# Performance work log

Hardware: AMD Instinct MI355X
Metric: run time of the kernel (lower is better)

Reference implementation:

```python
import jax, jax.numpy as jnp
import numpy as np

H, W, PART = 16, 16, 4
EPS = 1e-5


def _window_rows(h, part):
    # Static, boundary-clamped window row indices, as in position_aware_max.
    pr = h // part
    half = pr // 2
    idx = []
    for i in range(h):
        u, l = i - half, i + half
        if u < 0:
            u, l = 0, pr
        if l > h:
            u, l = h - pr, h
        idx.append(np.arange(u, l))
    return np.stack(idx)  # [h, pr] (uniform length since pr is even)


def _pam(s6, row_idx, dim):
    # s6: [p, g, hr, wr, hc, wc]; row index r = hr*W + wr, col index s = hc*W + wc.
    if dim == 0:
        # per column block i (hc == i): max over rows hr in window, all wr; keep wc
        sc = jnp.moveaxis(s6, 4, 0)  # [hc, p, g, hr, wr, wc]
        f = lambda sci, idx: jnp.take(sci, idx, axis=2).max(axis=(2, 3))
    else:
        # per row block i (hr == i): max over cols hc in window, all wc; keep wr
        sc = jnp.moveaxis(s6, 2, 0)  # [hr, p, g, wr, hc, wc]
        f = lambda sci, idx: jnp.take(sci, idx, axis=3).max(axis=(3, 4))
    out = jax.vmap(f)(sc, jnp.asarray(row_idx))  # [h, p, g, w]
    p, g = s6.shape[0], s6.shape[1]
    return jnp.transpose(out, (1, 2, 0, 3)).reshape(p, g, -1)  # [p, g, hw]


def _bn(x, gamma, beta, axes):
    # BatchNorm in training mode: biased batch statistics (torch default).
    m = x.mean(axis=axes, keepdims=True)
    v = x.var(axis=axes, keepdims=True)
    return gamma * (x - m) * jax.lax.rsqrt(v + EPS) + beta


def setup_inputs() -> dict:
    key = jax.random.key(0)
    k0, k1, k2 = jax.random.split(key, 3)
    p, g, c = 48, 48, 64
    hw = H * W
    return {
        "prob_fea": jax.random.normal(k0, (p, c, H, W), jnp.float32),
        "gal_fea": jax.random.normal(k1, (g, c, H, W), jnp.float32),
        "bn_gamma": jnp.ones((1,), jnp.float32),
        "bn_beta": jnp.zeros((1,), jnp.float32),
        "fc_w": jnp.full((1, hw), 1.0 / hw, jnp.float32),  # reset_parameters fill
        "fc_b": jax.random.normal(k2, (1,), jnp.float32) * 0.01,
        "lbn_gamma": jnp.ones((1,), jnp.float32),
        "lbn_beta": jnp.zeros((1,), jnp.float32),
    }


def reference(prob_fea, gal_fea, bn_gamma, bn_beta, fc_w, fc_b, lbn_gamma, lbn_beta):
    p, c = prob_fea.shape[0], prob_fea.shape[1]
    g = gal_fea.shape[0]
    hw = H * W
    pf = prob_fea.reshape(p, c, hw)
    gf = gal_fea.reshape(g, c, hw)
    score = jnp.einsum('pcs,gcr->pgrs', pf, gf)  # [p, g, hw, hw]
    s6 = score.reshape(p, g, H, W, H, W)
    row_idx = _window_rows(H, PART)
    s1 = _pam(s6, row_idx, 0)  # [p, g, hw]
    s2 = _pam(s6, row_idx, 1)  # [p, g, hw]
    sc = jnp.concatenate([s1, s2], axis=-1).reshape(-1, 1, hw)  # [2*p*g, 1, hw]
    sc = _bn(sc, bn_gamma, bn_beta, (0, 2)).reshape(-1, hw)
    sc = sc @ fc_w.T + fc_b  # [2*p*g, 1]
    sc = sc.reshape(-1, 2).sum(axis=1, keepdims=True)  # [p*g, 1]
    sc = _bn(sc, lbn_gamma, lbn_beta, (0,))
    return jax.nn.sigmoid(sc).reshape(p, g)
```

## Files before the change

### kernel.cpp

```cpp
#include <hip/hip_runtime.h>

typedef __attribute__((ext_vector_type(8))) short short8;
typedef __attribute__((ext_vector_type(4))) float float4v;

__constant__ unsigned short WIN[16] = {
    0x000F, 0x000F, 0x000F, 0x001E, 0x003C, 0x0078, 0x00F0, 0x01E0,
    0x03C0, 0x0780, 0x0F00, 0x1E00, 0x3C00, 0x7800, 0xF000, 0xF000
};
__constant__ int LO8[8] = {0, 0, 2, 4, 6, 8, 10, 12};
__constant__ int HI8[8] = {3, 5, 7, 9, 11, 13, 15, 15};

__device__ __forceinline__ unsigned short f2bf(float f) {
    unsigned int x = __builtin_bit_cast(unsigned int, f);
    x += 0x7FFF + ((x >> 16) & 1);
    return (unsigned short)(x >> 16);
}

struct __align__(16) U16x8 { unsigned short u[8]; };

__global__ __launch_bounds__(256) void pretranspose_kernel(
    const float* __restrict__ prob,
    const float* __restrict__ gal,
    unsigned short* __restrict__ outT)
{
    const int img = blockIdx.x;
    const float* src = (img < 48) ? (prob + img * 16384)
                                  : (gal + (img - 48) * 16384);
    unsigned short* dst = outT + img * 16384;
    const int tid = threadIdx.x;
    const int c0 = (tid & 7) * 8;
    const int s0 = (tid >> 3) * 8;
    unsigned short v[8][8];
#pragma unroll
    for (int i = 0; i < 8; ++i) {
        const float* p = src + (c0 + i) * 256 + s0;
        const float4v f0 = *(const float4v*)(p);
        const float4v f1 = *(const float4v*)(p + 4);
        v[i][0] = f2bf(f0.x); v[i][1] = f2bf(f0.y);
        v[i][2] = f2bf(f0.z); v[i][3] = f2bf(f0.w);
        v[i][4] = f2bf(f1.x); v[i][5] = f2bf(f1.y);
        v[i][6] = f2bf(f1.z); v[i][7] = f2bf(f1.w);
    }
#pragma unroll
    for (int j = 0; j < 8; ++j) {
        U16x8 o;
#pragma unroll
        for (int i = 0; i < 8; ++i) o.u[i] = v[i][j];
        const int srow = s0 + j;
        const int off = srow * 64 + (((c0 >> 3) ^ (srow & 7)) << 3);
        *(U16x8*)(dst + off) = o;
    }
}

__global__ __launch_bounds__(256, 3) void score_pam_kernel(
    const unsigned short* __restrict__ preT,
    const float* __restrict__ fcw,
    float* __restrict__ outDot,
    float* __restrict__ outSum,
    float* __restrict__ outSq)
{
    __shared__ unsigned short pfT[256 * 64];
    __shared__ unsigned short gfT[128 * 64];
    __shared__ float s1part[4 * 256];
    __shared__ float s2buf[256];

    const int tid = threadIdx.x;
    const int pair = blockIdx.x;
    const int ip = pair / 48;
    const int ig = pair % 48;
    const unsigned short* pimg = preT + ip * 16384;
    const unsigned short* gimg = preT + (48 + ig) * 16384;

    {
        float4v m = { -3.0e38f, -3.0e38f, -3.0e38f, -3.0e38f };
        *(float4v*)(s1part + tid * 4) = m;
    }
#pragma unroll
    for (int j = 0; j < 8; ++j) {
        const int off = j * 2048 + tid * 8;
        *(U16x8*)(pfT + off) = *(const U16x8*)(pimg + off);
    }

    const int lane = tid & 63;
    const int w = tid >> 6;
    const int laneM = lane & 15;
    const int q = lane >> 4;
    const int swzl = laneM & 7;

    for (int phase = 0; phase < 2; ++phase) {
        if (phase) __syncthreads();
#pragma unroll
        for (int j = 0; j < 4; ++j) {
            const int off = j * 2048 + tid * 8;
            *(U16x8*)(gfT + off) = *(const U16x8*)(gimg + phase * 8192 + off);
        }
        __syncthreads();

        const int t = phase * 4 + w;
        const int hr0 = 2 * t;
        const int hr1 = hr0 + 1;
        const int rl0 = 32 * w + laneM;
        const int rl1 = rl0 + 16;
        const short8 a00 = *(const short8*)(gfT + rl0 * 64 + ((q ^ swzl) << 3));
        const short8 a01 = *(const short8*)(gfT + rl0 * 64 + (((q + 4) ^ swzl) << 3));
        const short8 a10 = *(const short8*)(gfT + rl1 * 64 + ((q ^ swzl) << 3));
        const short8 a11 = *(const short8*)(gfT + rl1 * 64 + (((q + 4) ^ swzl) << 3));
        const unsigned int win0 = WIN[hr0];
        const unsigned int win1 = WIN[hr1];
        float4v s2r0 = { -3.0e38f, -3.0e38f, -3.0e38f, -3.0e38f };
        float4v s2r1 = s2r0;
        const int lo = LO8[t], hi = HI8[t];

        int sl = lo * 16 + laneM;
        short8 b0 = *(const short8*)(pfT + sl * 64 + ((q ^ swzl) << 3));
        short8 b1 = *(const short8*)(pfT + sl * 64 + (((q + 4) ^ swzl) << 3));
        for (int hc = lo; hc <= hi; ++hc) {
            const int hcn = (hc < hi) ? hc + 1 : hc;
            const int sln = hcn * 16 + laneM;
            const short8 nb0 = *(const short8*)(pfT + sln * 64 + ((q ^ swzl) << 3));
            const short8 nb1 = *(const short8*)(pfT + sln * 64 + (((q + 4) ^ swzl) << 3));

            float4v acc0 = { 0.f, 0.f, 0.f, 0.f };
            float4v acc1 = acc0;
            acc0 = __builtin_amdgcn_mfma_f32_16x16x32_bf16(a00, b0, acc0, 0, 0, 0);
            acc0 = __builtin_amdgcn_mfma_f32_16x16x32_bf16(a01, b1, acc0, 0, 0, 0);
            acc1 = __builtin_amdgcn_mfma_f32_16x16x32_bf16(a10, b0, acc1, 0, 0, 0);
            acc1 = __builtin_amdgcn_mfma_f32_16x16x32_bf16(a11, b1, acc1, 0, 0, 0);

            const bool s20 = (win0 >> hc) & 1;
            const bool s21 = (win1 >> hc) & 1;
            const unsigned int wc = WIN[hc];
            const bool s10 = (wc >> hr0) & 1;
            const bool s11 = (wc >> hr1) & 1;

            if (s20) {
                s2r0.x = fmaxf(s2r0.x, acc0.x); s2r0.y = fmaxf(s2r0.y, acc0.y);
                s2r0.z = fmaxf(s2r0.z, acc0.z); s2r0.w = fmaxf(s2r0.w, acc0.w);
            }
            if (s21) {
                s2r1.x = fmaxf(s2r1.x, acc1.x); s2r1.y = fmaxf(s2r1.y, acc1.y);
                s2r1.z = fmaxf(s2r1.z, acc1.z); s2r1.w = fmaxf(s2r1.w, acc1.w);
            }
            if (s10 || s11) {
                float vm = -3.0e38f;
                if (s10) vm = fmaxf(fmaxf(acc0.x, acc0.y), fmaxf(acc0.z, acc0.w));
                if (s11) vm = fmaxf(vm, fmaxf(fmaxf(acc1.x, acc1.y),
                                              fmaxf(acc1.z, acc1.w)));
                vm = fmaxf(vm, __shfl_xor(vm, 16, 64));
                vm = fmaxf(vm, __shfl_xor(vm, 32, 64));
                if (lane < 16) {
                    float* p = &s1part[w * 256 + hc * 16 + lane];
                    *p = fmaxf(*p, vm);
                }
            }
            b0 = nb0; b1 = nb1;
        }
#pragma unroll
        for (int d = 1; d < 16; d <<= 1) {
            s2r0.x = fmaxf(s2r0.x, __shfl_xor(s2r0.x, d, 64));
            s2r0.y = fmaxf(s2r0.y, __shfl_xor(s2r0.y, d, 64));
            s2r0.z = fmaxf(s2r0.z, __shfl_xor(s2r0.z, d, 64));
            s2r0.w = fmaxf(s2r0.w, __shfl_xor(s2r0.w, d, 64));
            s2r1.x = fmaxf(s2r1.x, __shfl_xor(s2r1.x, d, 64));
            s2r1.y = fmaxf(s2r1.y, __shfl_xor(s2r1.y, d, 64));
            s2r1.z = fmaxf(s2r1.z, __shfl_xor(s2r1.z, d, 64));
            s2r1.w = fmaxf(s2r1.w, __shfl_xor(s2r1.w, d, 64));
        }
        if (laneM == 0) {
            const int r0 = hr0 * 16 + q * 4;
            s2buf[r0 + 0] = s2r0.x; s2buf[r0 + 1] = s2r0.y;
            s2buf[r0 + 2] = s2r0.z; s2buf[r0 + 3] = s2r0.w;
            const int r1 = hr1 * 16 + q * 4;
            s2buf[r1 + 0] = s2r1.x; s2buf[r1 + 1] = s2r1.y;
            s2buf[r1 + 2] = s2r1.z; s2buf[r1 + 3] = s2r1.w;
        }
    }
    __syncthreads();

    {
        const float s1v = fmaxf(fmaxf(s1part[tid], s1part[256 + tid]),
                                fmaxf(s1part[512 + tid], s1part[768 + tid]));
        const float s2v = s2buf[tid];
        const float wj = fcw[tid];
        float dv = (s1v + s2v) * wj;
        float sv = s1v + s2v;
        float qv = s1v * s1v + s2v * s2v;
#pragma unroll
        for (int d = 32; d >= 1; d >>= 1) {
            dv += __shfl_down(dv, d, 64);
            sv += __shfl_down(sv, d, 64);
            qv += __shfl_down(qv, d, 64);
        }
        __syncthreads();
        if (lane == 0) {
            s2buf[w] = dv; s2buf[8 + w] = sv; s2buf[16 + w] = qv;
        }
        __syncthreads();
        if (tid == 0) {
            outDot[pair] = s2buf[0] + s2buf[1] + s2buf[2] + s2buf[3];
            outSum[pair] = s2buf[8] + s2buf[9] + s2buf[10] + s2buf[11];
            outSq[pair]  = s2buf[16] + s2buf[17] + s2buf[18] + s2buf[19];
        }
    }
}

__global__ __launch_bounds__(256) void finalize_kernel(
    const float* __restrict__ dDot,
    const float* __restrict__ dSum,
    const float* __restrict__ dSq,
    const float* __restrict__ bng,
    const float* __restrict__ bnb,
    const float* __restrict__ fcw,
    const float* __restrict__ fcb,
    const float* __restrict__ lg,
    const float* __restrict__ lb,
    float* __restrict__ outp)
{
    __shared__ float red[12];
    const int tid = threadIdx.x;
    const int lane = tid & 63;
    const int w = tid >> 6;

    float S = 0.f, Q = 0.f;
    float dv[9];
#pragma unroll
    for (int k = 0; k < 9; ++k) {
        const int i = tid + 256 * k;
        dv[k] = dDot[i];
        S += dSum[i];
        Q += dSq[i];
    }
    float Wj = fcw[tid];
#pragma unroll
    for (int d = 32; d >= 1; d >>= 1) {
        S += __shfl_down(S, d, 64);
        Q += __shfl_down(Q, d, 64);
        Wj += __shfl_down(Wj, d, 64);
    }
    if (lane == 0) { red[w] = S; red[4 + w] = Q; red[8 + w] = Wj; }
    __syncthreads();
    S = red[0] + red[1] + red[2] + red[3];
    Q = red[4] + red[5] + red[6] + red[7];
    const float W = red[8] + red[9] + red[10] + red[11];
    __syncthreads();

    const float N1 = 1179648.0f;
    const float m1 = S / N1;
    const float v1 = Q / N1 - m1 * m1;
    const float inv1 = rsqrtf(v1 + 1e-5f);
    const float g1 = bng[0], b1 = bnb[0], fb = fcb[0];
    const float g2 = lg[0], b2 = lb[0];
    const float cA = g1 * inv1;
    const float cB = 2.f * (b1 * W + fb) - cA * 2.f * m1 * W;

    float Sy = 0.f, Qy = 0.f;
    float yv[9];
#pragma unroll
    for (int k = 0; k < 9; ++k) {
        const float y = cA * dv[k] + cB;
        yv[k] = y;
        Sy += y;
        Qy += y * y;
    }
#pragma unroll
    for (int d = 32; d >= 1; d >>= 1) {
        Sy += __shfl_down(Sy, d, 64);
        Qy += __shfl_down(Qy, d, 64);
    }
    if (lane == 0) { red[w] = Sy; red[4 + w] = Qy; }
    __syncthreads();
    Sy = red[0] + red[1] + red[2] + red[3];
    Qy = red[4] + red[5] + red[6] + red[7];

    const float m2 = Sy / 2304.0f;
    const float v2 = Qy / 2304.0f - m2 * m2;
    const float inv2 = rsqrtf(v2 + 1e-5f);
#pragma unroll
    for (int k = 0; k < 9; ++k) {
        const int i = tid + 256 * k;
        const float z = g2 * (yv[k] - m2) * inv2 + b2;
        outp[i] = 1.0f / (1.0f + __expf(-z));
    }
}

extern "C" void kernel_launch(void* const* d_in, const int* in_sizes, int n_in,
                              void* d_out, int out_size, void* d_ws, size_t ws_size,
                              hipStream_t stream) {
    const float* prob = (const float*)d_in[0];
    const float* gal  = (const float*)d_in[1];
    const float* bng  = (const float*)d_in[2];
    const float* bnb  = (const float*)d_in[3];
    const float* fcw  = (const float*)d_in[4];
    const float* fcb  = (const float*)d_in[5];
    const float* lg   = (const float*)d_in[6];
    const float* lb   = (const float*)d_in[7];

    unsigned short* preT = (unsigned short*)d_ws;
    float* ws = (float*)((char*)d_ws + 96 * 16384 * sizeof(unsigned short));
    float* dDot = ws;
    float* dSum = ws + 2304;
    float* dSq  = ws + 4608;

    hipLaunchKernelGGL(pretranspose_kernel, dim3(96), dim3(256), 0, stream,
                       prob, gal, preT);
    hipLaunchKernelGGL(score_pam_kernel, dim3(48 * 48), dim3(256), 0, stream,
                       preT, fcw, dDot, dSum, dSq);
    hipLaunchKernelGGL(finalize_kernel, dim3(1), dim3(256), 0, stream,
                       dDot, dSum, dSq, bng, bnb, fcw, fcb, lg, lb,
                       (float*)d_out);
}
```

Measured before the change: 111.0 us.

## Compute PAM via symmetric two-pass window tiles with DPP row reductions

Restructures the score/PAM kernel so both max directions use the same code path. One pass stages the probe image in LDS and the other stages the gallery image, with A fragments loaded directly from global memory. This replaces the s1 cross-wave LDS partial-max scheme with per-row-tile running maxima. Those maxima are reduced with DPP row operations instead of shuffles, and the fc weights are staged in LDS. LDS use drops and launch bounds rise to 4 blocks per CU, which may recompute some overlapping MFMA tiles and cost registers.

```diff
diff --git a/kernel.cpp b/kernel.cpp
--- a/kernel.cpp
+++ b/kernel.cpp
@@ -3,12 +3,8 @@
 typedef __attribute__((ext_vector_type(8))) short short8;
 typedef __attribute__((ext_vector_type(4))) float float4v;
 
-__constant__ unsigned short WIN[16] = {
-    0x000F, 0x000F, 0x000F, 0x001E, 0x003C, 0x0078, 0x00F0, 0x01E0,
-    0x03C0, 0x0780, 0x0F00, 0x1E00, 0x3C00, 0x7800, 0xF000, 0xF000
-};
-__constant__ int LO8[8] = {0, 0, 2, 4, 6, 8, 10, 12};
-__constant__ int HI8[8] = {3, 5, 7, 9, 11, 13, 15, 15};
+__constant__ int LOW[16] = {0,0,0,1,2,3,4,5,6,7,8,9,10,11,12,12};
+__constant__ int HIW[16] = {3,3,3,4,5,6,7,8,9,10,11,12,13,14,15,15};
 
 __device__ __forceinline__ unsigned short f2bf(float f) {
     unsigned int x = __builtin_bit_cast(unsigned int, f);
@@ -17,6 +13,20 @@
 }
 
 struct __align__(16) U16x8 { unsigned short u[8]; };
+
+template <int CTRL>
+__device__ __forceinline__ float dppmaxf(float x) {
+    int y = __builtin_amdgcn_update_dpp(0, __builtin_bit_cast(int, x),
+                                        CTRL, 0xF, 0xF, true);
+    return fmaxf(x, __builtin_bit_cast(float, y));
+}
+__device__ __forceinline__ float rowmax16(float x) {
+    x = dppmaxf<0xB1>(x);
+    x = dppmaxf<0x4E>(x);
+    x = dppmaxf<0x141>(x);
+    x = dppmaxf<0x140>(x);
+    return x;
+}
 
 __global__ __launch_bounds__(256) void pretranspose_kernel(
     const float* __restrict__ prob,
@@ -52,17 +62,16 @@
     }
 }
 
-__global__ __launch_bounds__(256, 3) void score_pam_kernel(
+__global__ __launch_bounds__(256, 4) void score_pam_kernel(
     const unsigned short* __restrict__ preT,
     const float* __restrict__ fcw,
     float* __restrict__ outDot,
     float* __restrict__ outSum,
     float* __restrict__ outSq)
 {
-    __shared__ unsigned short pfT[256 * 64];
-    __shared__ unsigned short gfT[128 * 64];
-    __shared__ float s1part[4 * 256];
-    __shared__ float s2buf[256];
+    __shared__ unsigned short bufB[256 * 64];
+    __shared__ float fcw_lds[256];
+    __shared__ float red[4][4][4];
 
     const int tid = threadIdx.x;
     const int pair = blockIdx.x;
@@ -71,136 +80,98 @@
     const unsigned short* pimg = preT + ip * 16384;
     const unsigned short* gimg = preT + (48 + ig) * 16384;
 
-    {
-        float4v m = { -3.0e38f, -3.0e38f, -3.0e38f, -3.0e38f };
-        *(float4v*)(s1part + tid * 4) = m;
-    }
-#pragma unroll
-    for (int j = 0; j < 8; ++j) {
-        const int off = j * 2048 + tid * 8;
-        *(U16x8*)(pfT + off) = *(const U16x8*)(pimg + off);
-    }
+    fcw_lds[tid] = fcw[tid];
 
     const int lane = tid & 63;
     const int w = tid >> 6;
     const int laneM = lane & 15;
     const int q = lane >> 4;
-    const int swzl = laneM & 7;
-
-    for (int phase = 0; phase < 2; ++phase) {
-        if (phase) __syncthreads();
+    const int z = laneM & 7;
+
+    float dot = 0.f, sum = 0.f, sq = 0.f;
+    const float msk = (laneM == 0) ? 1.0f : 0.0f;
+
+    int lo[4], hi[4];
+#pragma unroll
+    for (int j = 0; j < 4; ++j) { lo[j] = LOW[4 * w + j]; hi[j] = HIW[4 * w + j]; }
+
+    for (int pass = 0; pass < 2; ++pass) {
+        const unsigned short* Bimg = pass ? gimg : pimg;
+        const unsigned short* Aimg = pass ? pimg : gimg;
+        if (pass) __syncthreads();
+#pragma unroll
+        for (int j = 0; j < 8; ++j) {
+            const int off = j * 2048 + tid * 8;
+            *(U16x8*)(bufB + off) = *(const U16x8*)(Bimg + off);
+        }
+
+        short8 a0[4], a1[4];
 #pragma unroll
         for (int j = 0; j < 4; ++j) {
-            const int off = j * 2048 + tid * 8;
-            *(U16x8*)(gfT + off) = *(const U16x8*)(gimg + phase * 8192 + off);
-        }
+            const int srow = (4 * w + j) * 16 + laneM;
+            a0[j] = *(const short8*)(Aimg + srow * 64 + ((q ^ z) << 3));
+            a1[j] = *(const short8*)(Aimg + srow * 64 + (((q + 4) ^ z) << 3));
+        }
+
+        float4v run[4];
+#pragma unroll
+        for (int j = 0; j < 4; ++j)
+            run[j] = (float4v){ -3.0e38f, -3.0e38f, -3.0e38f, -3.0e38f };
+
         __syncthreads();
 
-        const int t = phase * 4 + w;
-        const int hr0 = 2 * t;
-        const int hr1 = hr0 + 1;
-        const int rl0 = 32 * w + laneM;
-        const int rl1 = rl0 + 16;
-        const short8 a00 = *(const short8*)(gfT + rl0 * 64 + ((q ^ swzl) << 3));
-        const short8 a01 = *(const short8*)(gfT + rl0 * 64 + (((q + 4) ^ swzl) << 3));
-        const short8 a10 = *(const short8*)(gfT + rl1 * 64 + ((q ^ swzl) << 3));
-        const short8 a11 = *(const short8*)(gfT + rl1 * 64 + (((q + 4) ^ swzl) << 3));
-        const unsigned int win0 = WIN[hr0];
-        const unsigned int win1 = WIN[hr1];
-        float4v s2r0 = { -3.0e38f, -3.0e38f, -3.0e38f, -3.0e38f };
-        float4v s2r1 = s2r0;
-        const int lo = LO8[t], hi = HI8[t];
-
-        int sl = lo * 16 + laneM;
-        short8 b0 = *(const short8*)(pfT + sl * 64 + ((q ^ swzl) << 3));
-        short8 b1 = *(const short8*)(pfT + sl * 64 + (((q + 4) ^ swzl) << 3));
-        for (int hc = lo; hc <= hi; ++hc) {
-            const int hcn = (hc < hi) ? hc + 1 : hc;
-            const int sln = hcn * 16 + laneM;
-            const short8 nb0 = *(const short8*)(pfT + sln * 64 + ((q ^ swzl) << 3));
-            const short8 nb1 = *(const short8*)(pfT + sln * 64 + (((q + 4) ^ swzl) << 3));
-
-            float4v acc0 = { 0.f, 0.f, 0.f, 0.f };
-            float4v acc1 = acc0;
-            acc0 = __builtin_amdgcn_mfma_f32_16x16x32_bf16(a00, b0, acc0, 0, 0, 0);
-            acc0 = __builtin_amdgcn_mfma_f32_16x16x32_bf16(a01, b1, acc0, 0, 0, 0);
-            acc1 = __builtin_amdgcn_mfma_f32_16x16x32_bf16(a10, b0, acc1, 0, 0, 0);
-            acc1 = __builtin_amdgcn_mfma_f32_16x16x32_bf16(a11, b1, acc1, 0, 0, 0);
-
-            const bool s20 = (win0 >> hc) & 1;
-            const bool s21 = (win1 >> hc) & 1;
-            const unsigned int wc = WIN[hc];
-            const bool s10 = (wc >> hr0) & 1;
-            const bool s11 = (wc >> hr1) & 1;
-
-            if (s20) {
-                s2r0.x = fmaxf(s2r0.x, acc0.x); s2r0.y = fmaxf(s2r0.y, acc0.y);
-                s2r0.z = fmaxf(s2r0.z, acc0.z); s2r0.w = fmaxf(s2r0.w, acc0.w);
-            }
-            if (s21) {
-                s2r1.x = fmaxf(s2r1.x, acc1.x); s2r1.y = fmaxf(s2r1.y, acc1.y);
-                s2r1.z = fmaxf(s2r1.z, acc1.z); s2r1.w = fmaxf(s2r1.w, acc1.w);
-            }
-            if (s10 || s11) {
-                float vm = -3.0e38f;
-                if (s10) vm = fmaxf(fmaxf(acc0.x, acc0.y), fmaxf(acc0.z, acc0.w));
-                if (s11) vm = fmaxf(vm, fmaxf(fmaxf(acc1.x, acc1.y),
-                                              fmaxf(acc1.z, acc1.w)));
-                vm = fmaxf(vm, __shfl_xor(vm, 16, 64));
-                vm = fmaxf(vm, __shfl_xor(vm, 32, 64));
-                if (lane < 16) {
-                    float* p = &s1part[w * 256 + hc * 16 + lane];
-                    *p = fmaxf(*p, vm);
+        int sl = lo[0] * 16 + laneM;
+        short8 b0 = *(const short8*)(bufB + sl * 64 + ((q ^ z) << 3));
+        short8 b1 = *(const short8*)(bufB + sl * 64 + (((q + 4) ^ z) << 3));
+        for (int ct = lo[0]; ct <= hi[3]; ++ct) {
+            const int ctn = (ct < hi[3]) ? ct + 1 : ct;
+            const int sln = ctn * 16 + laneM;
+            const short8 nb0 = *(const short8*)(bufB + sln * 64 + ((q ^ z) << 3));
+            const short8 nb1 = *(const short8*)(bufB + sln * 64 + (((q + 4) ^ z) << 3));
+#pragma unroll
+            for (int j = 0; j < 4; ++j) {
+                if (ct >= lo[j] && ct <= hi[j]) {
+                    float4v acc = { 0.f, 0.f, 0.f, 0.f };
+                    acc = __builtin_amdgcn_mfma_f32_16x16x32_bf16(a0[j], b0, acc, 0, 0, 0);
+                    acc = __builtin_amdgcn_mfma_f32_16x16x32_bf16(a1[j], b1, acc, 0, 0, 0);
+                    run[j].x = fmaxf(run[j].x, acc.x);
+                    run[j].y = fmaxf(run[j].y, acc.y);
+                    run[j].z = fmaxf(run[j].z, acc.z);
+                    run[j].w = fmaxf(run[j].w, acc.w);
                 }
             }
             b0 = nb0; b1 = nb1;
         }
-#pragma unroll
-        for (int d = 1; d < 16; d <<= 1) {
-            s2r0.x = fmaxf(s2r0.x, __shfl_xor(s2r0.x, d, 64));
-            s2r0.y = fmaxf(s2r0.y, __shfl_xor(s2r0.y, d, 64));
-            s2r0.z = fmaxf(s2r0.z, __shfl_xor(s2r0.z, d, 64));
-            s2r0.w = fmaxf(s2r0.w, __shfl_xor(s2r0.w, d, 64));
-            s2r1.x = fmaxf(s2r1.x, __shfl_xor(s2r1.x, d, 64));
-            s2r1.y = fmaxf(s2r1.y, __shfl_xor(s2r1.y, d, 64));
-            s2r1.z = fmaxf(s2r1.z, __shfl_xor(s2r1.z, d, 64));
-            s2r1.w = fmaxf(s2r1.w, __shfl_xor(s2r1.w, d, 64));
-        }
-        if (laneM == 0) {
-            const int r0 = hr0 * 16 + q * 4;
-            s2buf[r0 + 0] = s2r0.x; s2buf[r0 + 1] = s2r0.y;
-            s2buf[r0 + 2] = s2r0.z; s2buf[r0 + 3] = s2r0.w;
-            const int r1 = hr1 * 16 + q * 4;
-            s2buf[r1 + 0] = s2r1.x; s2buf[r1 + 1] = s2r1.y;
-            s2buf[r1 + 2] = s2r1.z; s2buf[r1 + 3] = s2r1.w;
-        }
-    }
-    __syncthreads();
-
-    {
-        const float s1v = fmaxf(fmaxf(s1part[tid], s1part[256 + tid]),
-                                fmaxf(s1part[512 + tid], s1part[768 + tid]));
-        const float s2v = s2buf[tid];
-        const float wj = fcw[tid];
-        float dv = (s1v + s2v) * wj;
-        float sv = s1v + s2v;
-        float qv = s1v * s1v + s2v * s2v;
-#pragma unroll
-        for (int d = 32; d >= 1; d >>= 1) {
-            dv += __shfl_down(dv, d, 64);
-            sv += __shfl_down(sv, d, 64);
-            qv += __shfl_down(qv, d, 64);
-        }
-        __syncthreads();
-        if (lane == 0) {
-            s2buf[w] = dv; s2buf[8 + w] = sv; s2buf[16 + w] = qv;
-        }
-        __syncthreads();
-        if (tid == 0) {
-            outDot[pair] = s2buf[0] + s2buf[1] + s2buf[2] + s2buf[3];
-            outSum[pair] = s2buf[8] + s2buf[9] + s2buf[10] + s2buf[11];
-            outSq[pair]  = s2buf[16] + s2buf[17] + s2buf[18] + s2buf[19];
-        }
+
+#pragma unroll
+        for (int j = 0; j < 4; ++j) {
+            float rx = rowmax16(run[j].x);
+            float ry = rowmax16(run[j].y);
+            float rz = rowmax16(run[j].z);
+            float rw = rowmax16(run[j].w);
+            const int rt = 4 * w + j;
+            const float4v fw = *(const float4v*)(fcw_lds + rt * 16 + q * 4);
+            float t;
+            t = msk * rx; dot += t * fw.x; sum += t; sq += t * rx;
+            t = msk * ry; dot += t * fw.y; sum += t; sq += t * ry;
+            t = msk * rz; dot += t * fw.z; sum += t; sq += t * rz;
+            t = msk * rw; dot += t * fw.w; sum += t; sq += t * rw;
+        }
+    }
+
+    if (laneM == 0) {
+        red[w][q][0] = dot; red[w][q][1] = sum; red[w][q][2] = sq;
+    }
+    __syncthreads();
+    if (tid < 3) {
+        float s = 0.f;
+#pragma unroll
+        for (int a = 0; a < 4; ++a)
+#pragma unroll
+            for (int b = 0; b < 4; ++b) s += red[a][b][tid];
+        if (tid == 0) outDot[pair] = s;
+        else if (tid == 1) outSum[pair] = s;
+        else outSq[pair] = s;
     }
 }
 
```

New measurement: 102.6 us. -7.6%, faster.
